# Performance work log

Hardware: AMD Instinct MI355X
Metric: run time of the kernel (lower is better)

The kernel has to match this reference:

```python
import jax, jax.numpy as jnp
import numpy as np

N_HEADS = 12
HEAD_DIM = 64
EMB = 768


def setup_inputs() -> dict:
    key = jax.random.key(0)
    k1, k2, k3 = jax.random.split(key, 3)
    B, S = 4, 2048
    x = jax.random.normal(k1, (B, S, EMB), dtype=jnp.float32)
    # nn.Linear-style init scale ~ 1/sqrt(fan_in)
    w_qkv = jax.random.normal(k2, (EMB, 3 * N_HEADS * HEAD_DIM), dtype=jnp.float32) * (EMB ** -0.5)
    w_out = jax.random.normal(k3, (N_HEADS * HEAD_DIM, EMB), dtype=jnp.float32) * ((N_HEADS * HEAD_DIM) ** -0.5)
    b_out = jnp.zeros((EMB,), dtype=jnp.float32)
    return {"x": x, "w_qkv": w_qkv, "w_out": w_out, "b_out": b_out}


def reference(x, w_qkv, w_out, b_out):
    B, S, E = x.shape
    qkv = x @ w_qkv                                   # [B,S,3*H*D]
    q, k, v = jnp.split(qkv, 3, axis=-1)
    def to_heads(t):
        return t.reshape(B, S, N_HEADS, HEAD_DIM).transpose(0, 2, 1, 3)  # [B,H,S,D]
    q, k, v = to_heads(q), to_heads(k), to_heads(v)
    scores = jnp.einsum('bhqd,bhkd->bhqk', q, k) / (HEAD_DIM ** 0.5)     # [B,H,S,S]
    probs = jax.nn.softmax(scores, axis=-1)
    attn = jnp.einsum('bhqk,bhkd->bhqd', probs, v)                       # [B,H,S,D]
    attn = attn.transpose(0, 2, 1, 3).reshape(B, S, N_HEADS * HEAD_DIM)
    return attn @ w_out + b_out
```

## Files before the change

kernel.cpp:

```cpp
#include <hip/hip_runtime.h>
#include <stdint.h>

typedef unsigned short u16;
typedef __attribute__((ext_vector_type(8))) __bf16 bf16x8;
typedef __attribute__((ext_vector_type(4))) __bf16 bf16x4;
typedef __attribute__((ext_vector_type(8))) unsigned short u16x8;
typedef __attribute__((ext_vector_type(4))) float f32x4;

__device__ __forceinline__ void glds16(const u16* g, u16* l) {
  auto* gp = reinterpret_cast<const __attribute__((address_space(1))) unsigned*>(
      reinterpret_cast<uintptr_t>(g));
  auto* lp = reinterpret_cast<__attribute__((address_space(3))) unsigned*>(
      reinterpret_cast<uintptr_t>(l));
  __builtin_amdgcn_global_load_lds(gp, lp, 16, 0, 0);
}

__device__ __forceinline__ void pipe_bar() {
  asm volatile("s_waitcnt vmcnt(0) lgkmcnt(0)" ::: "memory");
  __builtin_amdgcn_s_barrier();
  asm volatile("" ::: "memory");
}

__device__ __forceinline__ void tp_tile(const float* __restrict__ src,
                                        u16* __restrict__ dst, int C, int Rd,
                                        int r0, int c0, float scale, u16* lds) {
  const int tid = threadIdx.x;
  {
    int r = tid >> 2, cb = (tid & 3) * 16;
#pragma unroll
    for (int k = 0; k < 4; ++k) {
      f32x4 v = *(const f32x4*)&src[(long)(r0 + r) * C + c0 + cb + k * 4];
      v = v * scale;
      *(bf16x4*)&lds[r * 72 + cb + k * 4] = __builtin_convertvector(v, bf16x4);
    }
  }
  __syncthreads();
  {
    int c = tid >> 2, rb = (tid & 3) * 16;
    u16x8 o0, o1;
#pragma unroll
    for (int q = 0; q < 8; ++q) {
      o0[q] = lds[(rb + q) * 72 + c];
      o1[q] = lds[(rb + 8 + q) * 72 + c];
    }
    *(u16x8*)&dst[(long)(c0 + c) * Rd + r0 + rb] = o0;
    *(u16x8*)&dst[(long)(c0 + c) * Rd + r0 + rb + 8] = o1;
  }
}

__global__ __launch_bounds__(256) void prep_k(const float* __restrict__ w_qkv,
                                              const float* __restrict__ w_out,
                                              const float* __restrict__ x,
                                              u16* __restrict__ wqkvT,
                                              u16* __restrict__ woutT,
                                              u16* __restrict__ xb) {
  __shared__ u16 lds[64 * 72];
  int bx = blockIdx.x;
  if (bx < 432) {
    int tr = bx / 36, tc = bx % 36;
    float sc = (tc < 12) ? 0.18033688011112042f : 1.0f;
    tp_tile(w_qkv, wqkvT, 2304, 768, tr * 64, tc * 64, sc, lds);
  } else if (bx < 576) {
    int t = bx - 432;
    tp_tile(w_out, woutT, 768, 768, (t / 12) * 64, (t % 12) * 64, 1.0f, lds);
  } else {
    int base = ((bx - 576) * 256 + (int)threadIdx.x) * 8;
#pragma unroll
    for (int it = 0; it < 16; ++it, base += 393216) {
      f32x4 a = *(const f32x4*)&x[base];
      f32x4 b = *(const f32x4*)&x[base + 4];
      *(bf16x4*)&xb[base] = __builtin_convertvector(a, bf16x4);
      *(bf16x4*)&xb[base + 4] = __builtin_convertvector(b, bf16x4);
    }
  }
}

template <bool OF32>
__device__ __forceinline__ void gemm_core(const u16* __restrict__ A,
                                          const u16* __restrict__ BT,
                                          void* __restrict__ Cv,
                                          const float* __restrict__ bias,
                                          int N, int K, int br, int bc,
                                          u16* As, u16* Bs) {
  const int tid = threadIdx.x;
  const int lane = tid & 63, wave = tid >> 6;
  const int quad = lane >> 4, l16 = lane & 15;
  const int wm = (wave >> 1) * 64, wn = (wave & 1) * 64;

  f32x4 acc[4][4] = {};

  const int srow = wave * 32 + (lane >> 2);
  const int scol = ((lane & 3) ^ ((lane >> 3) & 3)) * 8;
  const u16* ag = A + (long)(br + srow) * K + scol;
  const u16* bg = BT + (long)(bc + srow) * K + scol;
  const int rd = (quad ^ ((l16 >> 1) & 3)) * 8;

  glds16(ag, As + wave * 1024);
  glds16(ag + 16 * K, As + wave * 1024 + 512);
  glds16(bg, Bs + wave * 1024);
  glds16(bg + 16 * K, Bs + wave * 1024 + 512);
  pipe_bar();

  const int nk = K / 32;
#pragma unroll 2
  for (int kt = 0; kt < nk; ++kt) {
    const int pb = kt & 1;
    const u16* asc = As + pb * 4096;
    const u16* bsc = Bs + pb * 4096;
    if (kt + 1 < nk) {
      u16* asn = As + (pb ^ 1) * 4096;
      u16* bsn = Bs + (pb ^ 1) * 4096;
      const int k0 = (kt + 1) * 32;
      glds16(ag + k0, asn + wave * 1024);
      glds16(ag + k0 + 16 * K, asn + wave * 1024 + 512);
      glds16(bg + k0, bsn + wave * 1024);
      glds16(bg + k0 + 16 * K, bsn + wave * 1024 + 512);
    }
    bf16x8 af[4], bf[4];
#pragma unroll
    for (int i = 0; i < 4; ++i)
      af[i] = *(const bf16x8*)&asc[(wm + i * 16 + l16) * 32 + rd];
#pragma unroll
    for (int j = 0; j < 4; ++j)
      bf[j] = *(const bf16x8*)&bsc[(wn + j * 16 + l16) * 32 + rd];
    __builtin_amdgcn_s_setprio(1);
#pragma unroll
    for (int i = 0; i < 4; ++i)
#pragma unroll
      for (int j = 0; j < 4; ++j)
        acc[i][j] = __builtin_amdgcn_mfma_f32_16x16x32_bf16(af[i], bf[j],
                                                            acc[i][j], 0, 0, 0);
    __builtin_amdgcn_s_setprio(0);
    pipe_bar();
  }

#pragma unroll
  for (int i = 0; i < 4; ++i)
#pragma unroll
    for (int j = 0; j < 4; ++j)
#pragma unroll
      for (int r = 0; r < 4; ++r) {
        int row = br + wm + i * 16 + quad * 4 + r;
        int col = bc + wn + j * 16 + l16;
        float v = acc[i][j][r];
        if (OF32) {
          ((float*)Cv)[(long)row * N + col] = v + bias[col];
        } else {
          ((__bf16*)Cv)[(long)row * N + col] = (__bf16)v;
        }
      }
}

__global__ __launch_bounds__(256) void qkvt_k(const u16* __restrict__ xb,
                                              const u16* __restrict__ wqkvT,
                                              u16* __restrict__ qk,
                                              u16* __restrict__ vt) {
  __shared__ __align__(16) u16 As[2 * 128 * 32];
  __shared__ __align__(16) u16 Bs[2 * 128 * 32];
  int bx = blockIdx.x;
  if (bx < 768) {
    gemm_core<false>(xb, wqkvT, qk, nullptr, 1536, 768, (bx / 12) * 128,
                     (bx % 12) * 128, As, Bs);
  } else {
    int i = bx - 768;
    gemm_core<false>(wqkvT + 1536 * 768, xb, vt, nullptr, 8192, 768,
                     (i >> 6) * 128, (i & 63) * 128, As, Bs);
  }
}

__global__ __launch_bounds__(256) void gemm2_k(const u16* __restrict__ attnb,
                                               const u16* __restrict__ woutT,
                                               float* __restrict__ out,
                                               const float* __restrict__ bias) {
  __shared__ __align__(16) u16 As[2 * 128 * 32];
  __shared__ __align__(16) u16 Bs[2 * 128 * 32];
  gemm_core<true>(attnb, woutT, out, bias, 768, 768, blockIdx.y * 128,
                  blockIdx.x * 128, As, Bs);
}

__global__ __launch_bounds__(256, 3) void attn_k(const u16* __restrict__ qk,
                                                 const u16* __restrict__ vt,
                                                 u16* __restrict__ attnb) {
  const int LQ = 72;
  __shared__ __align__(16) u16 smem[16384 + 9216];
  u16* Ps = smem + 16384;

  const int tid = threadIdx.x;
  const int lane = tid & 63, wave = tid >> 6;
  const int quad = lane >> 4, l16 = lane & 15;
  const int qh = wave >> 1, sh = wave & 1;
  const int bid = blockIdx.x;
  const int xcd = bid & 7, slot = bid >> 3;
  const int bh = xcd * 6 + (slot >> 4);
  const int qt = slot & 15;
  const int bloc = bh / 12, h = bh % 12;
  const long rowbase = (long)bloc * 2048;

  const int trow = lane >> 3;
  const int tcol = ((lane & 7) ^ trow) * 8;
  const u16* kg = qk + (rowbase + wave * 16 + trow) * 1536 + 768 + h * 64 + tcol;
  const u16* vg = vt + (long)(h * 64 + wave * 16 + trow) * 8192 + rowbase + tcol;

  glds16(kg, smem + wave * 1024);
  glds16(kg + 8 * 1536, smem + wave * 1024 + 512);
  glds16(vg, smem + 8192 + wave * 1024);
  glds16(vg + 8 * 8192, smem + 8192 + wave * 1024 + 512);

#pragma unroll
  for (int it = 0; it < 4; ++it) {
    int c = tid + it * 256;
    int m = c >> 3, off = (c & 7) * 8;
    *(u16x8*)&Ps[m * LQ + off] =
        *(const u16x8*)&qk[(rowbase + qt * 128 + m) * 1536 + h * 64 + off];
  }
  __syncthreads();

  bf16x8 aq[2][4];
#pragma unroll
  for (int kk = 0; kk < 2; ++kk)
#pragma unroll
    for (int i = 0; i < 4; ++i)
      aq[kk][i] = *(const bf16x8*)&Ps[(qh * 64 + i * 16 + l16) * LQ + kk * 32 +
                                      quad * 8];

  bf16x8 ones;
#pragma unroll
  for (int q = 0; q < 8; ++q) ones[q] = (__bf16)1.0f;

  const int sw = l16 & 7;
  f32x4 o[4][4] = {};
  f32x4 l_acc[4] = {};

#pragma unroll 2
  for (int t = 0; t < 32; ++t) {
    const int pb = t & 1;
    const u16* ksc = smem + pb * 4096;
    const u16* vsc = smem + 8192 + pb * 4096;
    if (t < 31) {
      u16* ksn = smem + (pb ^ 1) * 4096;
      u16* vsn = smem + 8192 + (pb ^ 1) * 4096;
      const long kvK = (long)(t + 1) * 64 * 1536;
      const long kvV = (long)(t + 1) * 64;
      glds16(kg + kvK, ksn + wave * 1024);
      glds16(kg + kvK + 8 * 1536, ksn + wave * 1024 + 512);
      glds16(vg + kvV, vsn + wave * 1024);
      glds16(vg + kvV + 8 * 8192, vsn + wave * 1024 + 512);
    }

#pragma unroll
    for (int j = 0; j < 2; ++j) {
      bf16x8 bk0 = *(const bf16x8*)&ksc[(sh * 32 + j * 16 + l16) * 64 +
                                        (quad ^ sw) * 8];
      bf16x8 bk1 = *(const bf16x8*)&ksc[(sh * 32 + j * 16 + l16) * 64 +
                                        ((4 + quad) ^ sw) * 8];
      f32x4 sc[4] = {};
      __builtin_amdgcn_s_setprio(1);
#pragma unroll
      for (int i = 0; i < 4; ++i) {
        sc[i] = __builtin_amdgcn_mfma_f32_16x16x32_bf16(bk0, aq[0][i], sc[i],
                                                        0, 0, 0);
        sc[i] = __builtin_amdgcn_mfma_f32_16x16x32_bf16(bk1, aq[1][i], sc[i],
                                                        0, 0, 0);
      }
      __builtin_amdgcn_s_setprio(0);
#pragma unroll
      for (int i = 0; i < 4; ++i) {
        f32x4 p;
#pragma unroll
        for (int r = 0; r < 4; ++r)
          p[r] = __builtin_amdgcn_exp2f(sc[i][r]);
        *(bf16x4*)&Ps[(qh * 64 + i * 16 + l16) * LQ + sh * 32 + j * 16 +
                      quad * 4] = __builtin_convertvector(p, bf16x4);
      }
    }

    {
      bf16x8 bv[4];
#pragma unroll
      for (int n = 0; n < 4; ++n)
        bv[n] = *(const bf16x8*)&vsc[(n * 16 + l16) * 64 +
                                     ((sh * 4 + quad) ^ sw) * 8];
      __builtin_amdgcn_s_setprio(1);
#pragma unroll
      for (int i = 0; i < 4; ++i) {
        bf16x8 ap = *(const bf16x8*)&Ps[(qh * 64 + i * 16 + l16) * LQ +
                                        sh * 32 + quad * 8];
        l_acc[i] = __builtin_amdgcn_mfma_f32_16x16x32_bf16(ones, ap, l_acc[i],
                                                           0, 0, 0);
#pragma unroll
        for (int n = 0; n < 4; ++n)
          o[i][n] = __builtin_amdgcn_mfma_f32_16x16x32_bf16(ap, bv[n], o[i][n],
                                                            0, 0, 0);
      }
      __builtin_amdgcn_s_setprio(0);
    }

    pipe_bar();
  }

  float* Of = (float*)smem;
  float* Lp = (float*)&smem[16384];
  if (sh == 1) {
#pragma unroll
    for (int i = 0; i < 4; ++i) {
#pragma unroll
      for (int n = 0; n < 4; ++n)
#pragma unroll
        for (int r = 0; r < 4; ++r)
          Of[(qh * 64 + i * 16 + quad * 4 + r) * 64 + n * 16 + l16] =
              o[i][n][r];
      if (quad == 0) Lp[qh * 64 + i * 16 + l16] = l_acc[i][0];
    }
  }
  __syncthreads();
  if (sh == 0) {
#pragma unroll
    for (int i = 0; i < 4; ++i) {
      float lsum = l_acc[i][0] + Lp[qh * 64 + i * 16 + l16];
      f32x4 inv;
#pragma unroll
      for (int r = 0; r < 4; ++r)
        inv[r] = 1.0f / __shfl(lsum, quad * 4 + r, 64);
#pragma unroll
      for (int n = 0; n < 4; ++n)
#pragma unroll
        for (int r = 0; r < 4; ++r) {
          int srow = qt * 128 + qh * 64 + i * 16 + quad * 4 + r;
          float v = o[i][n][r] +
                    Of[(qh * 64 + i * 16 + quad * 4 + r) * 64 + n * 16 + l16];
          ((__bf16*)attnb)[(rowbase + srow) * 768 + h * 64 + n * 16 + l16] =
              (__bf16)(v * inv[r]);
        }
    }
  }
}

extern "C" void kernel_launch(void* const* d_in, const int* in_sizes, int n_in,
                              void* d_out, int out_size, void* d_ws,
                              size_t ws_size, hipStream_t stream) {
  const float* x = (const float*)d_in[0];
  const float* w_qkv = (const float*)d_in[1];
  const float* w_out = (const float*)d_in[2];
  const float* b_out = (const float*)d_in[3];
  float* out = (float*)d_out;

  char* ws = (char*)d_ws;
  u16* wqkvT = (u16*)(ws);
  u16* woutT = (u16*)(ws + 3538944);
  u16* vt = (u16*)(ws + 4718592);
  u16* xb = (u16*)(ws + 17301504);
  u16* attnb = xb;
  u16* qkb = (u16*)d_out;

  prep_k<<<768, 256, 0, stream>>>(w_qkv, w_out, x, wqkvT, woutT, xb);
  qkvt_k<<<1152, 256, 0, stream>>>(xb, wqkvT, qkb, vt);
  attn_k<<<768, 256, 0, stream>>>(qkb, vt, attnb);
  gemm2_k<<<dim3(6, 64), 256, 0, stream>>>(attnb, woutT, out, b_out);
}
```

Before: 215.5 us.

## Drop GEMM double buffering, load Q directly to registers, restructure attention inner loop

The GEMM core goes from a double-buffered global_load_lds pipeline to a single buffer with __syncthreads before and after each k-step, and the setprio hints are removed. This halves LDS use per block but no longer overlaps loads with MFMA. In the attention kernel, Q fragments are read straight from global memory into registers instead of being staged through LDS. The score MFMAs for both j halves are now issued together, with the V fragment loads hoisted ahead of the exp/store phase, to give the scheduler more independent work.

```diff
diff --git a/kernel.cpp b/kernel.cpp
--- a/kernel.cpp
+++ b/kernel.cpp
@@ -95,43 +95,26 @@
   const u16* bg = BT + (long)(bc + srow) * K + scol;
   const int rd = (quad ^ ((l16 >> 1) & 3)) * 8;
 
-  glds16(ag, As + wave * 1024);
-  glds16(ag + 16 * K, As + wave * 1024 + 512);
-  glds16(bg, Bs + wave * 1024);
-  glds16(bg + 16 * K, Bs + wave * 1024 + 512);
-  pipe_bar();
-
-  const int nk = K / 32;
-#pragma unroll 2
-  for (int kt = 0; kt < nk; ++kt) {
-    const int pb = kt & 1;
-    const u16* asc = As + pb * 4096;
-    const u16* bsc = Bs + pb * 4096;
-    if (kt + 1 < nk) {
-      u16* asn = As + (pb ^ 1) * 4096;
-      u16* bsn = Bs + (pb ^ 1) * 4096;
-      const int k0 = (kt + 1) * 32;
-      glds16(ag + k0, asn + wave * 1024);
-      glds16(ag + k0 + 16 * K, asn + wave * 1024 + 512);
-      glds16(bg + k0, bsn + wave * 1024);
-      glds16(bg + k0 + 16 * K, bsn + wave * 1024 + 512);
-    }
+  for (int k0 = 0; k0 < K; k0 += 32) {
+    glds16(ag + k0, As + wave * 1024);
+    glds16(ag + k0 + 16 * K, As + wave * 1024 + 512);
+    glds16(bg + k0, Bs + wave * 1024);
+    glds16(bg + k0 + 16 * K, Bs + wave * 1024 + 512);
+    __syncthreads();
     bf16x8 af[4], bf[4];
 #pragma unroll
     for (int i = 0; i < 4; ++i)
-      af[i] = *(const bf16x8*)&asc[(wm + i * 16 + l16) * 32 + rd];
+      af[i] = *(const bf16x8*)&As[(wm + i * 16 + l16) * 32 + rd];
 #pragma unroll
     for (int j = 0; j < 4; ++j)
-      bf[j] = *(const bf16x8*)&bsc[(wn + j * 16 + l16) * 32 + rd];
-    __builtin_amdgcn_s_setprio(1);
+      bf[j] = *(const bf16x8*)&Bs[(wn + j * 16 + l16) * 32 + rd];
 #pragma unroll
     for (int i = 0; i < 4; ++i)
 #pragma unroll
       for (int j = 0; j < 4; ++j)
         acc[i][j] = __builtin_amdgcn_mfma_f32_16x16x32_bf16(af[i], bf[j],
                                                             acc[i][j], 0, 0, 0);
-    __builtin_amdgcn_s_setprio(0);
-    pipe_bar();
+    __syncthreads();
   }
 
 #pragma unroll
@@ -155,8 +138,8 @@
                                               const u16* __restrict__ wqkvT,
                                               u16* __restrict__ qk,
                                               u16* __restrict__ vt) {
-  __shared__ __align__(16) u16 As[2 * 128 * 32];
-  __shared__ __align__(16) u16 Bs[2 * 128 * 32];
+  __shared__ __align__(16) u16 As[128 * 32];
+  __shared__ __align__(16) u16 Bs[128 * 32];
   int bx = blockIdx.x;
   if (bx < 768) {
     gemm_core<false>(xb, wqkvT, qk, nullptr, 1536, 768, (bx / 12) * 128,
@@ -172,8 +155,8 @@
                                                const u16* __restrict__ woutT,
                                                float* __restrict__ out,
                                                const float* __restrict__ bias) {
-  __shared__ __align__(16) u16 As[2 * 128 * 32];
-  __shared__ __align__(16) u16 Bs[2 * 128 * 32];
+  __shared__ __align__(16) u16 As[128 * 32];
+  __shared__ __align__(16) u16 Bs[128 * 32];
   gemm_core<true>(attnb, woutT, out, bias, 768, 768, blockIdx.y * 128,
                   blockIdx.x * 128, As, Bs);
 }
@@ -206,21 +189,13 @@
   glds16(vg, smem + 8192 + wave * 1024);
   glds16(vg + 8 * 8192, smem + 8192 + wave * 1024 + 512);
 
-#pragma unroll
-  for (int it = 0; it < 4; ++it) {
-    int c = tid + it * 256;
-    int m = c >> 3, off = (c & 7) * 8;
-    *(u16x8*)&Ps[m * LQ + off] =
-        *(const u16x8*)&qk[(rowbase + qt * 128 + m) * 1536 + h * 64 + off];
-  }
-  __syncthreads();
-
   bf16x8 aq[2][4];
 #pragma unroll
   for (int kk = 0; kk < 2; ++kk)
 #pragma unroll
     for (int i = 0; i < 4; ++i)
-      aq[kk][i] = *(const bf16x8*)&Ps[(qh * 64 + i * 16 + l16) * LQ + kk * 32 +
+      aq[kk][i] = *(const bf16x8*)&qk[(rowbase + qt * 128 + qh * 64 + i * 16 +
+                                       l16) * 1536 + h * 64 + kk * 32 +
                                       quad * 8];
 
   bf16x8 ones;
@@ -230,6 +205,8 @@
   const int sw = l16 & 7;
   f32x4 o[4][4] = {};
   f32x4 l_acc[4] = {};
+
+  pipe_bar();
 
 #pragma unroll 2
   for (int t = 0; t < 32; ++t) {
@@ -247,53 +224,59 @@
       glds16(vg + kvV + 8 * 8192, vsn + wave * 1024 + 512);
     }
 
+    f32x4 sc[2][4];
+    bf16x8 bk[2][2];
 #pragma unroll
     for (int j = 0; j < 2; ++j) {
-      bf16x8 bk0 = *(const bf16x8*)&ksc[(sh * 32 + j * 16 + l16) * 64 +
-                                        (quad ^ sw) * 8];
-      bf16x8 bk1 = *(const bf16x8*)&ksc[(sh * 32 + j * 16 + l16) * 64 +
-                                        ((4 + quad) ^ sw) * 8];
-      f32x4 sc[4] = {};
-      __builtin_amdgcn_s_setprio(1);
+      bk[j][0] = *(const bf16x8*)&ksc[(sh * 32 + j * 16 + l16) * 64 +
+                                      (quad ^ sw) * 8];
+      bk[j][1] = *(const bf16x8*)&ksc[(sh * 32 + j * 16 + l16) * 64 +
+                                      ((4 + quad) ^ sw) * 8];
+    }
+    __builtin_amdgcn_s_setprio(1);
+#pragma unroll
+    for (int j = 0; j < 2; ++j)
 #pragma unroll
       for (int i = 0; i < 4; ++i) {
-        sc[i] = __builtin_amdgcn_mfma_f32_16x16x32_bf16(bk0, aq[0][i], sc[i],
-                                                        0, 0, 0);
-        sc[i] = __builtin_amdgcn_mfma_f32_16x16x32_bf16(bk1, aq[1][i], sc[i],
-                                                        0, 0, 0);
+        f32x4 z = {0.0f, 0.0f, 0.0f, 0.0f};
+        z = __builtin_amdgcn_mfma_f32_16x16x32_bf16(bk[j][0], aq[0][i], z,
+                                                    0, 0, 0);
+        sc[j][i] = __builtin_amdgcn_mfma_f32_16x16x32_bf16(bk[j][1], aq[1][i],
+                                                           z, 0, 0, 0);
       }
-      __builtin_amdgcn_s_setprio(0);
+    __builtin_amdgcn_s_setprio(0);
+
+    bf16x8 bv[4];
+#pragma unroll
+    for (int n = 0; n < 4; ++n)
+      bv[n] = *(const bf16x8*)&vsc[(n * 16 + l16) * 64 +
+                                   ((sh * 4 + quad) ^ sw) * 8];
+
+#pragma unroll
+    for (int j = 0; j < 2; ++j)
 #pragma unroll
       for (int i = 0; i < 4; ++i) {
         f32x4 p;
 #pragma unroll
         for (int r = 0; r < 4; ++r)
-          p[r] = __builtin_amdgcn_exp2f(sc[i][r]);
+          p[r] = __builtin_amdgcn_exp2f(sc[j][i][r]);
         *(bf16x4*)&Ps[(qh * 64 + i * 16 + l16) * LQ + sh * 32 + j * 16 +
                       quad * 4] = __builtin_convertvector(p, bf16x4);
       }
-    }
-
-    {
-      bf16x8 bv[4];
+
+    __builtin_amdgcn_s_setprio(1);
+#pragma unroll
+    for (int i = 0; i < 4; ++i) {
+      bf16x8 ap = *(const bf16x8*)&Ps[(qh * 64 + i * 16 + l16) * LQ +
+                                      sh * 32 + quad * 8];
+      l_acc[i] = __builtin_amdgcn_mfma_f32_16x16x32_bf16(ones, ap, l_acc[i],
+                                                         0, 0, 0);
 #pragma unroll
       for (int n = 0; n < 4; ++n)
-        bv[n] = *(const bf16x8*)&vsc[(n * 16 + l16) * 64 +
-                                     ((sh * 4 + quad) ^ sw) * 8];
-      __builtin_amdgcn_s_setprio(1);
-#pragma unroll
-      for (int i = 0; i < 4; ++i) {
-        bf16x8 ap = *(const bf16x8*)&Ps[(qh * 64 + i * 16 + l16) * LQ +
-                                        sh * 32 + quad * 8];
-        l_acc[i] = __builtin_amdgcn_mfma_f32_16x16x32_bf16(ones, ap, l_acc[i],
-                                                           0, 0, 0);
-#pragma unroll
-        for (int n = 0; n < 4; ++n)
-          o[i][n] = __builtin_amdgcn_mfma_f32_16x16x32_bf16(ap, bv[n], o[i][n],
-                                                            0, 0, 0);
-      }
-      __builtin_amdgcn_s_setprio(0);
-    }
+        o[i][n] = __builtin_amdgcn_mfma_f32_16x16x32_bf16(ap, bv[n], o[i][n],
+                                                          0, 0, 0);
+    }
+    __builtin_amdgcn_s_setprio(0);
 
     pipe_bar();
   }
```

Result: slower. 260.5 us (+20.9%).
